# Kernel tuning notes

Measured on AMD Instinct MI355X. Metric: run time of the kernel, lower is better.

The kernel has to match this reference:

```python
import jax, jax.numpy as jnp
import numpy as np

D = 512
H = 8
DH = D // H
EPS = 1e-5


def layer_norm(x, gamma, beta):
    mu = jnp.mean(x, axis=-1, keepdims=True)
    var = jnp.mean(jnp.square(x - mu), axis=-1, keepdims=True)
    return (x - mu) * jax.lax.rsqrt(var + EPS) * gamma + beta


def setup_inputs() -> dict:
    key = jax.random.key(0)
    ks = jax.random.split(key, 16)
    B, N = 16, 1024
    s = 1.0 / np.sqrt(D)
    return {
        "h": jax.random.normal(ks[0], (B, N, D), jnp.float32),
        "ln1_g": jnp.ones((D,), jnp.float32),
        "ln1_b": jnp.zeros((D,), jnp.float32),
        "wq": jax.random.normal(ks[1], (D, D), jnp.float32) * s,
        "bq": jnp.zeros((D,), jnp.float32),
        "wk": jax.random.normal(ks[2], (D, D), jnp.float32) * s,
        "bk": jnp.zeros((D,), jnp.float32),
        "wv": jax.random.normal(ks[3], (D, D), jnp.float32) * s,
        "bv": jnp.zeros((D,), jnp.float32),
        "wo": jax.random.normal(ks[4], (D, D), jnp.float32) * s,
        "bo": jnp.zeros((D,), jnp.float32),
        "ln2_g": jnp.ones((D,), jnp.float32),
        "ln2_b": jnp.zeros((D,), jnp.float32),
        "w1": jax.random.normal(ks[5], (2 * D, D), jnp.float32) * s,
        "b1": jnp.zeros((2 * D,), jnp.float32),
        "w2": jax.random.normal(ks[6], (D, 2 * D), jnp.float32) * (1.0 / np.sqrt(2 * D)),
        "b2": jnp.zeros((D,), jnp.float32),
    }


def reference(h, ln1_g, ln1_b, wq, bq, wk, bk, wv, bv, wo, bo,
              ln2_g, ln2_b, w1, b1, w2, b2):
    B, N, _ = h.shape
    hn = layer_norm(h, ln1_g, ln1_b)
    # projections (torch Linear convention: x @ W^T + b)
    q = (hn @ wq.T + bq).reshape(B, N, H, DH)
    k = (hn @ wk.T + bk).reshape(B, N, H, DH)
    v = (hn @ wv.T + bv).reshape(B, N, H, DH)
    scores = jnp.einsum("bqhd,bkhd->bhqk", q, k) / np.sqrt(DH)
    attn = jax.nn.softmax(scores, axis=-1)  # [B,H,N,N]
    ctx = jnp.einsum("bhqk,bkhd->bqhd", attn, v).reshape(B, N, D)
    attn_out = ctx @ wo.T + bo
    # averaged attention weights (torch default average_attn_weights=True)
    attn_weights = jnp.mean(attn, axis=1)  # [B,N,N]
    h = h + attn_out
    # FFN: LN -> Linear(d,2d) -> SiLU -> Linear(2d,d), residual
    f = layer_norm(h, ln2_g, ln2_b)
    f = jax.nn.silu(f @ w1.T + b1) @ w2.T + b2
    h = h + f
    return h, attn_weights
```

## Files before the change

kernel.cpp:

```cpp
#include <hip/hip_runtime.h>

typedef unsigned short u16;
typedef __attribute__((ext_vector_type(8))) short short8;
typedef __attribute__((ext_vector_type(4))) float floatx4;
typedef __attribute__((ext_vector_type(16))) float floatx16;

#define MFMA_BF16(a, b, c) __builtin_amdgcn_mfma_f32_16x16x32_bf16((a), (b), (c), 0, 0, 0)
#define MFMA32(a, b, c) __builtin_amdgcn_mfma_f32_32x32x16_bf16((a), (b), (c), 0, 0, 0)

__device__ __forceinline__ u16 f2bf(float f) {
  unsigned b = __float_as_uint(f);
  b = b + 0x7FFFu + ((b >> 16) & 1u);
  return (u16)(b >> 16);
}

__device__ __forceinline__ float fexp8(float s) {
  float r;
  asm("v_exp_f32 %0, %1" : "=v"(r) : "v"(s * 0.18033688011112042f));
  return r;
}

__device__ __forceinline__ unsigned cvtpk(float a, float b) {
  unsigned r;
  asm("v_cvt_pk_bf16_f32 %0, %1, %2" : "=v"(r) : "v"(a), "v"(b));
  return r;
}

__device__ __forceinline__ void plswap(unsigned& x, unsigned& y) {
  asm("v_permlane32_swap_b32 %0, %1" : "+v"(x), "+v"(y));
}

__device__ __forceinline__ void gll16(const u16* g, u16* lds_uniform) {
  __builtin_amdgcn_global_load_lds(
      (const __attribute__((address_space(1))) void*)g,
      (__attribute__((address_space(3))) void*)lds_uniform, 16, 0, 0);
}

__global__ __launch_bounds__(256) void cast4_kernel(const float* __restrict__ src,
                                                    u16* __restrict__ dst, int n4) {
  int i = blockIdx.x * 256 + threadIdx.x;
  if (i < n4) {
    float4 v = ((const float4*)src)[i];
    ushort4 o;
    o.x = f2bf(v.x); o.y = f2bf(v.y); o.z = f2bf(v.z); o.w = f2bf(v.w);
    ((ushort4*)dst)[i] = o;
  }
}

__global__ __launch_bounds__(128) void ln_kernel(const float* __restrict__ x,
                                                 const float* __restrict__ g,
                                                 const float* __restrict__ be,
                                                 u16* __restrict__ y) {
  int row = blockIdx.x, t = threadIdx.x;
  float4 v = ((const float4*)(x + (size_t)row * 512))[t];
  float s = v.x + v.y + v.z + v.w;
  float q = v.x * v.x + v.y * v.y + v.z * v.z + v.w * v.w;
#pragma unroll
  for (int off = 32; off > 0; off >>= 1) {
    s += __shfl_xor(s, off);
    q += __shfl_xor(q, off);
  }
  __shared__ float sb[2], qb[2];
  int w = t >> 6;
  if ((t & 63) == 0) { sb[w] = s; qb[w] = q; }
  __syncthreads();
  s = sb[0] + sb[1];
  q = qb[0] + qb[1];
  float mu = s * (1.0f / 512.0f);
  float var = q * (1.0f / 512.0f) - mu * mu;
  float rs = rsqrtf(var + 1e-5f);
  float4 gg = ((const float4*)g)[t];
  float4 bb = ((const float4*)be)[t];
  ushort4 o;
  o.x = f2bf((v.x - mu) * rs * gg.x + bb.x);
  o.y = f2bf((v.y - mu) * rs * gg.y + bb.y);
  o.z = f2bf((v.z - mu) * rs * gg.z + bb.z);
  o.w = f2bf((v.w - mu) * rs * gg.w + bb.w);
  ((ushort4*)(y + (size_t)row * 512))[t] = o;
}

template <bool OUTB, bool SILU, bool RES>
__global__ __launch_bounds__(256) void gemm_bt_kernel(
    const u16* __restrict__ A, const u16* __restrict__ W,
    const float* __restrict__ bias, const float* __restrict__ res,
    void* __restrict__ out, int N, int K) {
  __shared__ __align__(16) u16 As[128 * 32];
  __shared__ __align__(16) u16 Bs[128 * 32];
  int t = threadIdx.x;
  int lane = t & 63, wave = t >> 6;
  int l15 = lane & 15, quad = lane >> 4;
  int rowBlk = blockIdx.y * 128, colBlk = blockIdx.x * 128;
  const u16* Ag = A + (size_t)(rowBlk + (t >> 2)) * K + (t & 3) * 8;
  const u16* Wg = W + (size_t)(colBlk + (t >> 2)) * K + (t & 3) * 8;
  u16* AsW = As + wave * 512;
  u16* BsW = Bs + wave * 512;
  int arow = (wave >> 1) * 64;
  int brow = (wave & 1) * 64;
  floatx4 acc[4][4] = {};
  for (int k0 = 0; k0 < K; k0 += 32) {
    gll16(Ag + k0, AsW);
    gll16(Ag + (size_t)64 * K + k0, AsW + 2048);
    gll16(Wg + k0, BsW);
    gll16(Wg + (size_t)64 * K + k0, BsW + 2048);
    __syncthreads();
    short8 a[4], b[4];
#pragma unroll
    for (int i = 0; i < 4; ++i)
      a[i] = *(const short8*)(As + (size_t)(arow + i * 16 + l15) * 32 + quad * 8);
#pragma unroll
    for (int j = 0; j < 4; ++j)
      b[j] = *(const short8*)(Bs + (size_t)(brow + j * 16 + l15) * 32 + quad * 8);
#pragma unroll
    for (int i = 0; i < 4; ++i)
#pragma unroll
      for (int j = 0; j < 4; ++j)
        acc[i][j] = MFMA_BF16(a[i], b[j], acc[i][j]);
    __syncthreads();
  }
#pragma unroll
  for (int j = 0; j < 4; ++j) {
    int col = colBlk + brow + j * 16 + l15;
    float bs = bias[col];
#pragma unroll
    for (int i = 0; i < 4; ++i) {
      int row0 = rowBlk + arow + i * 16 + quad * 4;
#pragma unroll
      for (int r = 0; r < 4; ++r) {
        size_t idx = (size_t)(row0 + r) * N + col;
        float v = acc[i][j][r] + bs;
        if (RES) v += res[idx];
        if (SILU) v = v * (1.0f / (1.0f + __expf(-v)));
        if (OUTB) ((u16*)out)[idx] = f2bf(v);
        else ((float*)out)[idx] = v;
      }
    }
  }
}

__global__ __launch_bounds__(256) void vtrans_kernel(const u16* __restrict__ qkv,
                                                     u16* __restrict__ vT) {
  __shared__ u16 tile[64][68];
  int blk = blockIdx.x;
  int b = blk >> 7, h = (blk >> 4) & 7, n0 = (blk & 15) * 64;
  int t = threadIdx.x;
#pragma unroll
  for (int rep = 0; rep < 16; ++rep) {
    int idx = t + rep * 256;
    int nl = idx >> 6, dh = idx & 63;
    tile[nl][dh] = qkv[(size_t)(b * 1024 + n0 + nl) * 1536 + 1024 + h * 64 + dh];
  }
  __syncthreads();
#pragma unroll
  for (int rep = 0; rep < 16; ++rep) {
    int idx = t + rep * 256;
    int dh = idx >> 6, nl = idx & 63;
    vT[((size_t)(b * 8 + h) * 64 + dh) * 1024 + n0 + nl] = tile[nl][dh];
  }
}

__global__ __launch_bounds__(256, 4) void attn_ctx_kernel(const u16* __restrict__ qkv,
                                                          const u16* __restrict__ vT,
                                                          u16* __restrict__ ctx,
                                                          float* __restrict__ linv_g) {
  __shared__ __align__(16) u16 Kb[2][4096];
  __shared__ __align__(16) u16 Vb[2][4096];
  int t = threadIdx.x, lane = t & 63, wave = t >> 6;
  int l31 = lane & 31, hi = lane >> 5;
  int li = lane >> 3, sl = lane & 7;
  int bid = blockIdx.x;
  int L = (bid & 7) * 128 + (bid >> 3);
  int qblk = L & 7, h = (L >> 3) & 7, b = L >> 6;
  int q0w = qblk * 128 + wave * 32;

  short8 qf[4];
  const u16* qbase = qkv + (size_t)(b * 1024 + q0w + l31) * 1536 + h * 64;
#pragma unroll
  for (int t4 = 0; t4 < 4; ++t4)
    qf[t4] = *(const short8*)(qbase + t4 * 16 + hi * 8);

  short8 ones;
#pragma unroll
  for (int i = 0; i < 8; ++i) ones[i] = (short)0x3F80;

  floatx16 oacc[2] = {};
  floatx16 psum = {};

  const u16* ksec = qkv + (size_t)(b * 1024) * 1536 + 512 + h * 64;
  const u16* vsec = vT + ((size_t)(b * 8 + h) * 64) * 1024;

  auto stageKV = [&](int c, u16* kbuf, u16* vbuf) {
#pragma unroll
    for (int j = 0; j < 2; ++j) {
      int r0 = wave * 16 + j * 8;
      int row = r0 + li;
      gll16(ksec + (size_t)(c * 64 + row) * 1536 + ((sl ^ (row & 7)) << 3),
            kbuf + r0 * 64);
      gll16(vsec + (size_t)row * 1024 + c * 64 + ((sl ^ (row & 7)) << 3),
            vbuf + r0 * 64);
    }
  };

  stageKV(0, Kb[0], Vb[0]);
  __syncthreads();

#pragma unroll 1
  for (int c = 0; c < 16; ++c) {
    int bf = c & 1;
    if (c < 15) stageKV(c + 1, Kb[bf ^ 1], Vb[bf ^ 1]);
    short8 pa[4];
#pragma unroll
    for (int ct = 0; ct < 2; ++ct) {
      floatx16 s = {};
#pragma unroll
      for (int t4 = 0; t4 < 4; ++t4) {
        int key = ct * 32 + l31;
        int g2 = t4 * 2 + hi;
        short8 kf = *(const short8*)&Kb[bf][key * 64 + ((g2 ^ (key & 7)) << 3)];
        s = MFMA32(kf, qf[t4], s);
      }
#pragma unroll
      for (int r = 0; r < 16; ++r) s[r] = fexp8(s[r]);
#pragma unroll
      for (int j = 0; j < 2; ++j) {
        unsigned a0 = cvtpk(s[j * 8 + 0], s[j * 8 + 1]);
        unsigned b0 = cvtpk(s[j * 8 + 4], s[j * 8 + 5]);
        unsigned a1 = cvtpk(s[j * 8 + 2], s[j * 8 + 3]);
        unsigned b1 = cvtpk(s[j * 8 + 6], s[j * 8 + 7]);
        plswap(a0, b0);
        plswap(a1, b1);
        union { unsigned u[4]; short8 v8; } uu;
        uu.u[0] = a0; uu.u[1] = a1; uu.u[2] = b0; uu.u[3] = b1;
        pa[ct * 2 + j] = uu.v8;
      }
    }
#pragma unroll
    for (int ks = 0; ks < 4; ++ks) {
      psum = MFMA32(pa[ks], ones, psum);
#pragma unroll
      for (int ct2 = 0; ct2 < 2; ++ct2) {
        int dh = ct2 * 32 + l31;
        int kg = ks * 2 + hi;
        short8 vf = *(const short8*)&Vb[bf][dh * 64 + ((kg ^ (dh & 7)) << 3)];
        oacc[ct2] = MFMA32(pa[ks], vf, oacc[ct2]);
      }
    }
    __syncthreads();
  }

  float il[16];
#pragma unroll
  for (int r = 0; r < 16; ++r) il[r] = 1.0f / psum[r];
  if (l31 == 0) {
#pragma unroll
    for (int reg = 0; reg < 16; ++reg) {
      int row = (reg & 3) + 8 * (reg >> 2) + 4 * hi;
      linv_g[(size_t)(b * 8 + h) * 1024 + q0w + row] = il[reg];
    }
  }
#pragma unroll
  for (int ct = 0; ct < 2; ++ct)
#pragma unroll
    for (int reg = 0; reg < 16; ++reg) {
      int row = (reg & 3) + 8 * (reg >> 2) + 4 * hi;
      ctx[(size_t)(b * 1024 + q0w + row) * 512 + h * 64 + ct * 32 + l31] =
          f2bf(oacc[ct][reg] * il[reg]);
    }
}

__global__ __launch_bounds__(256, 4) void attn_avg_kernel(const u16* __restrict__ qkv,
                                                          const float* __restrict__ linv_g,
                                                          float* __restrict__ attnw) {
  __shared__ __align__(16) u16 Qs[128 * 64];
  __shared__ __align__(16) u16 Ks[64 * 64];
  int t = threadIdx.x, lane = t & 63, wave = t >> 6;
  int l31 = lane & 31, hi = lane >> 5;
  int bid = blockIdx.x;
  int L = (bid & 7) * 256 + (bid >> 3);
  int b = L >> 7;
  int r7 = L & 127;
  int kq = r7 & 15, qb = r7 >> 4;
  int q0 = qb * 128;
  int q0w = q0 + wave * 32;
  int key0 = kq * 64;

  int li = lane >> 3, sl = lane & 7;

  floatx16 acc0 = {}, acc1 = {};

#pragma unroll 1
  for (int h = 0; h < 8; ++h) {
    {
      const u16* qsec = qkv + (size_t)(b * 1024 + q0) * 1536 + h * 64;
#pragma unroll
      for (int j = 0; j < 4; ++j) {
        int r0 = wave * 32 + j * 8;
        int row = r0 + li;
        gll16(qsec + (size_t)row * 1536 + ((sl ^ (row & 7)) << 3), Qs + r0 * 64);
      }
      const u16* ksec = qkv + (size_t)(b * 1024 + key0) * 1536 + 512 + h * 64;
#pragma unroll
      for (int j = 0; j < 2; ++j) {
        int r0 = wave * 16 + j * 8;
        int row = r0 + li;
        gll16(ksec + (size_t)row * 1536 + ((sl ^ (row & 7)) << 3), Ks + r0 * 64);
      }
    }
    __syncthreads();

    const float* lg = linv_g + (size_t)(b * 8 + h) * 1024 + q0w + 4 * hi;
    float4 il0 = *(const float4*)(lg);
    float4 il1 = *(const float4*)(lg + 8);
    float4 il2 = *(const float4*)(lg + 16);
    float4 il3 = *(const float4*)(lg + 24);
    float il[16] = {il0.x, il0.y, il0.z, il0.w, il1.x, il1.y, il1.z, il1.w,
                    il2.x, il2.y, il2.z, il2.w, il3.x, il3.y, il3.z, il3.w};

    short8 qf[4];
#pragma unroll
    for (int t4 = 0; t4 < 4; ++t4) {
      int row = wave * 32 + l31;
      int g2 = t4 * 2 + hi;
      qf[t4] = *(const short8*)(Qs + row * 64 + ((g2 ^ (row & 7)) << 3));
    }
#pragma unroll
    for (int ct = 0; ct < 2; ++ct) {
      floatx16 sacc = {};
#pragma unroll
      for (int t4 = 0; t4 < 4; ++t4) {
        int key = ct * 32 + l31;
        int g2 = t4 * 2 + hi;
        short8 kf = *(const short8*)(Ks + key * 64 + ((g2 ^ (key & 7)) << 3));
        sacc = MFMA32(qf[t4], kf, sacc);
      }
      if (ct == 0) {
#pragma unroll
        for (int r = 0; r < 16; ++r) acc0[r] += fexp8(sacc[r]) * il[r];
      } else {
#pragma unroll
        for (int r = 0; r < 16; ++r) acc1[r] += fexp8(sacc[r]) * il[r];
      }
    }
    __syncthreads();
  }

#pragma unroll
  for (int r = 0; r < 16; ++r) {
    int row = (r & 3) + 8 * (r >> 2) + 4 * hi;
    float* dst = &attnw[(size_t)(b * 1024 + q0w + row) * 1024 + key0 + l31];
    __builtin_nontemporal_store(acc0[r] * 0.125f, dst);
    __builtin_nontemporal_store(acc1[r] * 0.125f, dst + 32);
  }
}

extern "C" void kernel_launch(void* const* d_in, const int* in_sizes, int n_in,
                              void* d_out, int out_size, void* d_ws, size_t ws_size,
                              hipStream_t stream) {
  (void)in_sizes; (void)n_in; (void)out_size; (void)ws_size;
  const float* h   = (const float*)d_in[0];
  const float* g1  = (const float*)d_in[1];
  const float* be1 = (const float*)d_in[2];
  const float* wq  = (const float*)d_in[3];
  const float* bq  = (const float*)d_in[4];
  const float* wk  = (const float*)d_in[5];
  const float* bk  = (const float*)d_in[6];
  const float* wv  = (const float*)d_in[7];
  const float* bv  = (const float*)d_in[8];
  const float* wo  = (const float*)d_in[9];
  const float* bo  = (const float*)d_in[10];
  const float* g2  = (const float*)d_in[11];
  const float* be2 = (const float*)d_in[12];
  const float* w1  = (const float*)d_in[13];
  const float* b1  = (const float*)d_in[14];
  const float* w2  = (const float*)d_in[15];
  const float* b2  = (const float*)d_in[16];

  char* p = (char*)d_ws;
  auto carve = [&](size_t bytes) {
    char* r = p;
    p += (bytes + 255) & ~(size_t)255;
    return r;
  };
  u16*   wcat = (u16*)carve((size_t)1536 * 512 * 2);
  u16*   wob  = (u16*)carve((size_t)512 * 512 * 2);
  u16*   w1b  = (u16*)carve((size_t)1024 * 512 * 2);
  u16*   w2b  = (u16*)carve((size_t)512 * 1024 * 2);
  float* bcat = (float*)carve((size_t)1536 * 4);
  u16*   hn   = (u16*)carve((size_t)16384 * 512 * 2);
  u16*   qkvb = (u16*)carve((size_t)16384 * 1536 * 2);
  u16*   vTb  = (u16*)carve((size_t)16384 * 512 * 2);
  u16*   ctxb = (u16*)carve((size_t)16384 * 512 * 2);
  u16*   fb   = (u16*)carve((size_t)16384 * 512 * 2);
  u16*   gb   = (u16*)carve((size_t)16384 * 1024 * 2);
  float* linv = (float*)carve((size_t)16 * 8 * 1024 * 4);

  float* outh = (float*)d_out;
  float* outattn = outh + (size_t)16384 * 512;

  cast4_kernel<<<256, 256, 0, stream>>>(wq, wcat, 65536);
  cast4_kernel<<<256, 256, 0, stream>>>(wk, wcat + 512 * 512, 65536);
  cast4_kernel<<<256, 256, 0, stream>>>(wv, wcat + 2 * 512 * 512, 65536);
  cast4_kernel<<<256, 256, 0, stream>>>(wo, wob, 65536);
  cast4_kernel<<<512, 256, 0, stream>>>(w1, w1b, 131072);
  cast4_kernel<<<512, 256, 0, stream>>>(w2, w2b, 131072);
  hipMemcpyAsync(bcat, bq, 512 * 4, hipMemcpyDeviceToDevice, stream);
  hipMemcpyAsync(bcat + 512, bk, 512 * 4, hipMemcpyDeviceToDevice, stream);
  hipMemcpyAsync(bcat + 1024, bv, 512 * 4, hipMemcpyDeviceToDevice, stream);

  ln_kernel<<<16384, 128, 0, stream>>>(h, g1, be1, hn);
  gemm_bt_kernel<true, false, false><<<dim3(12, 128), 256, 0, stream>>>(
      hn, wcat, bcat, nullptr, qkvb, 1536, 512);
  vtrans_kernel<<<2048, 256, 0, stream>>>(qkvb, vTb);
  attn_ctx_kernel<<<1024, 256, 0, stream>>>(qkvb, vTb, ctxb, linv);
  attn_avg_kernel<<<2048, 256, 0, stream>>>(qkvb, linv, outattn);
  gemm_bt_kernel<false, false, true><<<dim3(4, 128), 256, 0, stream>>>(
      ctxb, wob, bo, h, outh, 512, 512);
  ln_kernel<<<16384, 128, 0, stream>>>(outh, g2, be2, fb);
  gemm_bt_kernel<true, true, false><<<dim3(8, 128), 256, 0, stream>>>(
      fb, w1b, b1, nullptr, gb, 1024, 512);
  gemm_bt_kernel<false, false, true><<<dim3(4, 128), 256, 0, stream>>>(
      gb, w2b, b2, outh, outh, 512, 1024);
}
```

Before: 416.7 us.

## Batch weight casts, remap GEMM blocks per XCD, widen avg-attn key tile, add setprio

Six weight-cast launches and three bias memcpys are merged into one cast kernel and one bias-concat kernel, cutting launch overhead. GEMM blocks move to a 1D grid with an XCD-aware remap so blocks sharing rows land on the same chiplet for L2 reuse. The averaged-attention kernel doubles its key tile to 128 keys per block, so Q is loaded half as often, at the cost of more LDS and registers. s_setprio hints are placed around MFMA sections in the attention context kernel to improve overlap between waves.

```diff
diff --git a/kernel.cpp b/kernel.cpp
--- a/kernel.cpp
+++ b/kernel.cpp
@@ -36,15 +36,41 @@
       (__attribute__((address_space(3))) void*)lds_uniform, 16, 0, 0);
 }
 
-__global__ __launch_bounds__(256) void cast4_kernel(const float* __restrict__ src,
-                                                    u16* __restrict__ dst, int n4) {
+__global__ __launch_bounds__(256) void cast_all_kernel(
+    const float* __restrict__ wq, const float* __restrict__ wk,
+    const float* __restrict__ wv, const float* __restrict__ wo,
+    const float* __restrict__ w1, const float* __restrict__ w2,
+    u16* __restrict__ wcat, u16* __restrict__ wob,
+    u16* __restrict__ w1b, u16* __restrict__ w2b) {
   int i = blockIdx.x * 256 + threadIdx.x;
-  if (i < n4) {
-    float4 v = ((const float4*)src)[i];
-    ushort4 o;
-    o.x = f2bf(v.x); o.y = f2bf(v.y); o.z = f2bf(v.z); o.w = f2bf(v.w);
-    ((ushort4*)dst)[i] = o;
-  }
+  const float4* src;
+  ushort4* dst;
+  if (i < 196608) {
+    src = (const float4*)((i < 65536) ? wq : (i < 131072) ? wk : wv) + (i & 65535);
+    dst = (ushort4*)wcat + i;
+  } else if (i < 262144) {
+    src = (const float4*)wo + (i - 196608);
+    dst = (ushort4*)wob + (i - 196608);
+  } else if (i < 393216) {
+    src = (const float4*)w1 + (i - 262144);
+    dst = (ushort4*)w1b + (i - 262144);
+  } else {
+    src = (const float4*)w2 + (i - 393216);
+    dst = (ushort4*)w2b + (i - 393216);
+  }
+  float4 v = *src;
+  ushort4 o;
+  o.x = f2bf(v.x); o.y = f2bf(v.y); o.z = f2bf(v.z); o.w = f2bf(v.w);
+  *dst = o;
+}
+
+__global__ __launch_bounds__(256) void bias_cat_kernel(const float* __restrict__ bq,
+                                                       const float* __restrict__ bk,
+                                                       const float* __restrict__ bv,
+                                                       float* __restrict__ bcat) {
+  int i = blockIdx.x * 256 + threadIdx.x;
+  float v = (i < 512) ? bq[i] : (i < 1024) ? bk[i - 512] : bv[i - 1024];
+  bcat[i] = v;
 }
 
 __global__ __launch_bounds__(128) void ln_kernel(const float* __restrict__ x,
@@ -83,13 +109,15 @@
 __global__ __launch_bounds__(256) void gemm_bt_kernel(
     const u16* __restrict__ A, const u16* __restrict__ W,
     const float* __restrict__ bias, const float* __restrict__ res,
-    void* __restrict__ out, int N, int K) {
+    void* __restrict__ out, int N, int K, int nx) {
   __shared__ __align__(16) u16 As[128 * 32];
   __shared__ __align__(16) u16 Bs[128 * 32];
   int t = threadIdx.x;
   int lane = t & 63, wave = t >> 6;
   int l15 = lane & 15, quad = lane >> 4;
-  int rowBlk = blockIdx.y * 128, colBlk = blockIdx.x * 128;
+  int nblk = gridDim.x;
+  int L = (blockIdx.x & 7) * (nblk >> 3) + (blockIdx.x >> 3);
+  int rowBlk = (L / nx) * 128, colBlk = (L % nx) * 128;
   const u16* Ag = A + (size_t)(rowBlk + (t >> 2)) * K + (t & 3) * 8;
   const u16* Wg = W + (size_t)(colBlk + (t >> 2)) * K + (t & 3) * 8;
   u16* AsW = As + wave * 512;
@@ -211,6 +239,7 @@
 #pragma unroll
     for (int ct = 0; ct < 2; ++ct) {
       floatx16 s = {};
+      __builtin_amdgcn_s_setprio(1);
 #pragma unroll
       for (int t4 = 0; t4 < 4; ++t4) {
         int key = ct * 32 + l31;
@@ -218,6 +247,7 @@
         short8 kf = *(const short8*)&Kb[bf][key * 64 + ((g2 ^ (key & 7)) << 3)];
         s = MFMA32(kf, qf[t4], s);
       }
+      __builtin_amdgcn_s_setprio(0);
 #pragma unroll
       for (int r = 0; r < 16; ++r) s[r] = fexp8(s[r]);
 #pragma unroll
@@ -233,6 +263,7 @@
         pa[ct * 2 + j] = uu.v8;
       }
     }
+    __builtin_amdgcn_s_setprio(1);
 #pragma unroll
     for (int ks = 0; ks < 4; ++ks) {
       psum = MFMA32(pa[ks], ones, psum);
@@ -244,6 +275,7 @@
         oacc[ct2] = MFMA32(pa[ks], vf, oacc[ct2]);
       }
     }
+    __builtin_amdgcn_s_setprio(0);
     __syncthreads();
   }
 
@@ -271,39 +303,31 @@
                                                           const float* __restrict__ linv_g,
                                                           float* __restrict__ attnw) {
   __shared__ __align__(16) u16 Qs[128 * 64];
-  __shared__ __align__(16) u16 Ks[64 * 64];
+  __shared__ __align__(16) u16 Ks[128 * 64];
   int t = threadIdx.x, lane = t & 63, wave = t >> 6;
   int l31 = lane & 31, hi = lane >> 5;
+  int li = lane >> 3, sl = lane & 7;
   int bid = blockIdx.x;
-  int L = (bid & 7) * 256 + (bid >> 3);
-  int b = L >> 7;
-  int r7 = L & 127;
-  int kq = r7 & 15, qb = r7 >> 4;
+  int L = (bid & 7) * 128 + (bid >> 3);
+  int b = L >> 6;
+  int r6 = L & 63;
+  int kq = r6 & 7, qb = r6 >> 3;
   int q0 = qb * 128;
   int q0w = q0 + wave * 32;
-  int key0 = kq * 64;
-
-  int li = lane >> 3, sl = lane & 7;
-
-  floatx16 acc0 = {}, acc1 = {};
+  int key0 = kq * 128;
+
+  floatx16 acc[4] = {};
 
 #pragma unroll 1
   for (int h = 0; h < 8; ++h) {
-    {
-      const u16* qsec = qkv + (size_t)(b * 1024 + q0) * 1536 + h * 64;
-#pragma unroll
-      for (int j = 0; j < 4; ++j) {
-        int r0 = wave * 32 + j * 8;
-        int row = r0 + li;
-        gll16(qsec + (size_t)row * 1536 + ((sl ^ (row & 7)) << 3), Qs + r0 * 64);
-      }
-      const u16* ksec = qkv + (size_t)(b * 1024 + key0) * 1536 + 512 + h * 64;
-#pragma unroll
-      for (int j = 0; j < 2; ++j) {
-        int r0 = wave * 16 + j * 8;
-        int row = r0 + li;
-        gll16(ksec + (size_t)row * 1536 + ((sl ^ (row & 7)) << 3), Ks + r0 * 64);
-      }
+    const u16* qsec = qkv + (size_t)(b * 1024 + q0) * 1536 + h * 64;
+    const u16* ksec = qkv + (size_t)(b * 1024 + key0) * 1536 + 512 + h * 64;
+#pragma unroll
+    for (int j = 0; j < 4; ++j) {
+      int r0 = wave * 32 + j * 8;
+      int row = r0 + li;
+      gll16(qsec + (size_t)row * 1536 + ((sl ^ (row & 7)) << 3), Qs + r0 * 64);
+      gll16(ksec + (size_t)row * 1536 + ((sl ^ (row & 7)) << 3), Ks + r0 * 64);
     }
     __syncthreads();
 
@@ -323,7 +347,7 @@
       qf[t4] = *(const short8*)(Qs + row * 64 + ((g2 ^ (row & 7)) << 3));
     }
 #pragma unroll
-    for (int ct = 0; ct < 2; ++ct) {
+    for (int ct = 0; ct < 4; ++ct) {
       floatx16 sacc = {};
 #pragma unroll
       for (int t4 = 0; t4 < 4; ++t4) {
@@ -332,13 +356,8 @@
         short8 kf = *(const short8*)(Ks + key * 64 + ((g2 ^ (key & 7)) << 3));
         sacc = MFMA32(qf[t4], kf, sacc);
       }
-      if (ct == 0) {
-#pragma unroll
-        for (int r = 0; r < 16; ++r) acc0[r] += fexp8(sacc[r]) * il[r];
-      } else {
-#pragma unroll
-        for (int r = 0; r < 16; ++r) acc1[r] += fexp8(sacc[r]) * il[r];
-      }
+#pragma unroll
+      for (int r = 0; r < 16; ++r) acc[ct][r] += fexp8(sacc[r]) * il[r];
     }
     __syncthreads();
   }
@@ -347,8 +366,9 @@
   for (int r = 0; r < 16; ++r) {
     int row = (r & 3) + 8 * (r >> 2) + 4 * hi;
     float* dst = &attnw[(size_t)(b * 1024 + q0w + row) * 1024 + key0 + l31];
-    __builtin_nontemporal_store(acc0[r] * 0.125f, dst);
-    __builtin_nontemporal_store(acc1[r] * 0.125f, dst + 32);
+#pragma unroll
+    for (int ct = 0; ct < 4; ++ct)
+      __builtin_nontemporal_store(acc[ct][r] * 0.125f, dst + ct * 32);
   }
 }
 
@@ -396,27 +416,21 @@
   float* outh = (float*)d_out;
   float* outattn = outh + (size_t)16384 * 512;
 
-  cast4_kernel<<<256, 256, 0, stream>>>(wq, wcat, 65536);
-  cast4_kernel<<<256, 256, 0, stream>>>(wk, wcat + 512 * 512, 65536);
-  cast4_kernel<<<256, 256, 0, stream>>>(wv, wcat + 2 * 512 * 512, 65536);
-  cast4_kernel<<<256, 256, 0, stream>>>(wo, wob, 65536);
-  cast4_kernel<<<512, 256, 0, stream>>>(w1, w1b, 131072);
-  cast4_kernel<<<512, 256, 0, stream>>>(w2, w2b, 131072);
-  hipMemcpyAsync(bcat, bq, 512 * 4, hipMemcpyDeviceToDevice, stream);
-  hipMemcpyAsync(bcat + 512, bk, 512 * 4, hipMemcpyDeviceToDevice, stream);
-  hipMemcpyAsync(bcat + 1024, bv, 512 * 4, hipMemcpyDeviceToDevice, stream);
+  cast_all_kernel<<<2048, 256, 0, stream>>>(wq, wk, wv, wo, w1, w2,
+                                            wcat, wob, w1b, w2b);
+  bias_cat_kernel<<<6, 256, 0, stream>>>(bq, bk, bv, bcat);
 
   ln_kernel<<<16384, 128, 0, stream>>>(h, g1, be1, hn);
-  gemm_bt_kernel<true, false, false><<<dim3(12, 128), 256, 0, stream>>>(
-      hn, wcat, bcat, nullptr, qkvb, 1536, 512);
+  gemm_bt_kernel<true, false, false><<<1536, 256, 0, stream>>>(
+      hn, wcat, bcat, nullptr, qkvb, 1536, 512, 12);
   vtrans_kernel<<<2048, 256, 0, stream>>>(qkvb, vTb);
   attn_ctx_kernel<<<1024, 256, 0, stream>>>(qkvb, vTb, ctxb, linv);
-  attn_avg_kernel<<<2048, 256, 0, stream>>>(qkvb, linv, outattn);
-  gemm_bt_kernel<false, false, true><<<dim3(4, 128), 256, 0, stream>>>(
-      ctxb, wob, bo, h, outh, 512, 512);
+  attn_avg_kernel<<<1024, 256, 0, stream>>>(qkvb, linv, outattn);
+  gemm_bt_kernel<false, false, true><<<512, 256, 0, stream>>>(
+      ctxb, wob, bo, h, outh, 512, 512, 4);
   ln_kernel<<<16384, 128, 0, stream>>>(outh, g2, be2, fb);
-  gemm_bt_kernel<true, true, false><<<dim3(8, 128), 256, 0, stream>>>(
-      fb, w1b, b1, nullptr, gb, 1024, 512);
-  gemm_bt_kernel<false, false, true><<<dim3(4, 128), 256, 0, stream>>>(
-      gb, w2b, b2, outh, outh, 512, 1024);
-}
+  gemm_bt_kernel<true, true, false><<<1024, 256, 0, stream>>>(
+      fb, w1b, b1, nullptr, gb, 1024, 512, 8);
+  gemm_bt_kernel<false, false, true><<<512, 256, 0, stream>>>(
+      gb, w2b, b2, outh, outh, 512, 1024, 4);
+}
```

New measurement: 467.0 us. +12.1%, slower.
